# Performance work log

Measured on AMD Instinct MI355X. Metric: run time of the kernel, lower is better.

The kernel has to match this reference:

```python
import jax, jax.numpy as jnp
import numpy as np

N, E, IN, HID, HEADS, OUT = 50000, 800000, 128, 64, 4, 64


def setup_inputs() -> dict:
    key = jax.random.key(0)
    ks = jax.random.split(key, 13)
    s1 = 1.0 / np.sqrt(IN)
    s2 = 1.0 / np.sqrt(HID * HEADS)
    s3 = 1.0 / np.sqrt(HID)
    return {
        'x': jax.random.normal(ks[0], (N, IN), dtype=jnp.float32),
        'edge_index': jax.random.randint(ks[1], (2, E), 0, N, dtype=jnp.int64),
        # GATv2 layer 1: heads=HEADS, out=HID, concat=True
        'W1l': jax.random.normal(ks[2], (IN, HEADS * HID), dtype=jnp.float32) * s1,
        'W1r': jax.random.normal(ks[3], (IN, HEADS * HID), dtype=jnp.float32) * s1,
        'att1': jax.random.normal(ks[4], (HEADS, HID), dtype=jnp.float32) * s3,
        'b1': jnp.zeros((HEADS * HID,), dtype=jnp.float32),
        # GATv2 layer 2: heads=1, out=HID
        'W2l': jax.random.normal(ks[5], (HEADS * HID, HID), dtype=jnp.float32) * s2,
        'W2r': jax.random.normal(ks[6], (HEADS * HID, HID), dtype=jnp.float32) * s2,
        'att2': jax.random.normal(ks[7], (1, HID), dtype=jnp.float32) * s3,
        'b2': jnp.zeros((HID,), dtype=jnp.float32),
        # final Linear(HID, OUT)
        'Wlin': jax.random.normal(ks[8], (HID, OUT), dtype=jnp.float32) * s3,
        'blin': jnp.zeros((OUT,), dtype=jnp.float32),
    }


def _gatv2(x, src, dst, Wl, Wr, att, bias, n):
    # PyG GATv2Conv (share_weights=False): x_j -> lin_l, x_i -> lin_r
    H, C = att.shape
    xl = (x @ Wl).reshape(n, H, C)  # source transform [N,H,C]
    xr = (x @ Wr).reshape(n, H, C)  # destination transform [N,H,C]
    # per-edge GATv2 score: a^T LeakyReLU(xl_j + xr_i)
    e = jnp.sum(jax.nn.leaky_relu(xl[src] + xr[dst], 0.2) * att, axis=-1)  # [E,H]
    # scatter-softmax over edges sharing a destination
    m = jax.ops.segment_max(e, dst, num_segments=n)  # [N,H]
    ex = jnp.exp(e - m[dst])
    denom = jax.ops.segment_sum(ex, dst, num_segments=n)
    alpha = ex / (denom[dst] + 1e-16)  # [E,H]
    # weighted scatter-add aggregation of source features
    out = jax.ops.segment_sum(xl[src] * alpha[:, :, None], dst, num_segments=n)  # [N,H,C]
    return out.reshape(n, H * C) + bias


def reference(x, edge_index, W1l, W1r, att1, b1, W2l, W2r, att2, b2, Wlin, blin):
    n = x.shape[0]
    loops = jnp.arange(n, dtype=edge_index.dtype)
    src = jnp.concatenate([edge_index[0], loops])  # add_self_loops=True (PyG default)
    dst = jnp.concatenate([edge_index[1], loops])
    h = _gatv2(x, src, dst, W1l, W1r, att1, b1, n)
    h = jax.nn.elu(h)
    h = _gatv2(h, src, dst, W2l, W2r, att2, b2, n)
    h = jax.nn.elu(h)
    return h @ Wlin + blin
```

## Files before the change

kernel.cpp:

```cpp
#include <hip/hip_runtime.h>
#include <hip/hip_bf16.h>
#include <math.h>

#define N_NODES 50000
#define N_EDGES 800000
#define ETOT (N_EDGES + N_NODES)
#define NGRP 196
#define HBLK 416

typedef __attribute__((ext_vector_type(8))) short short8;
typedef __attribute__((ext_vector_type(4))) float floatx4;
typedef __attribute__((ext_vector_type(2))) float f32x2;

__device__ __forceinline__ float bf_lo(unsigned u) { return __uint_as_float(u << 16); }
__device__ __forceinline__ float bf_hi(unsigned u) { return __uint_as_float(u & 0xffff0000u); }
__device__ __forceinline__ unsigned short f2bf(float f) {
    unsigned u = __float_as_uint(f);
    return (unsigned short)((u + 0x7fffu + ((u >> 16) & 1u)) >> 16);
}
__device__ __forceinline__ unsigned pack2bf(float a, float b) {
    return (unsigned)f2bf(a) | ((unsigned)f2bf(b) << 16);
}
#define DPP_ADD(p, ctrl) \
    (p) += __int_as_float(__builtin_amdgcn_update_dpp(0, __float_as_int(p), (ctrl), 0xF, 0xF, true))

__global__ __launch_bounds__(256) void k_prep(const float* __restrict__ W1l,
                                              const float* __restrict__ W1r,
                                              const float* __restrict__ W2l,
                                              const float* __restrict__ W2r,
                                              const float* __restrict__ Wlin,
                                              unsigned short* __restrict__ Wt1,
                                              unsigned short* __restrict__ Wt2,
                                              unsigned short* __restrict__ Wt3,
                                              const int* __restrict__ ei,
                                              unsigned* __restrict__ part) {
    __shared__ unsigned sh[256];
    const int b = blockIdx.x;
    const int t = threadIdx.x;
    if (b < 400) {
        const int idx = b * 256 + t;
        if (idx < 65536) {
            const int k = idx >> 9;
            const int n = idx & 511;
            const float v = (n < 256) ? W1l[k * 256 + n] : W1r[k * 256 + (n - 256)];
            Wt1[n * 128 + k] = f2bf(v);
        } else if (idx < 98304) {
            const int j = idx - 65536;
            const int k = j >> 7;
            const int n = j & 127;
            const float v = (n < 64) ? W2l[k * 64 + n] : W2r[k * 64 + (n - 64)];
            Wt2[n * 256 + k] = f2bf(v);
        } else {
            const int j = idx - 98304;
            const int n = j >> 6, k = j & 63;
            Wt3[n * 64 + k] = f2bf(Wlin[k * 64 + n]);
        }
        return;
    }
    const int bb = b - 400;
    sh[t] = 0;
    __syncthreads();
#pragma unroll
    for (int j = 0; j < 8; j++) {
        const int e = bb * 2048 + j * 256 + t;
        if (e < ETOT) {
            const int d = (e < N_EDGES) ? ei[N_EDGES + e] : (e - N_EDGES);
            atomicAdd(&sh[d >> 8], 1u);
        }
    }
    __syncthreads();
    part[bb * 256 + t] = sh[t];
}

__global__ __launch_bounds__(256) void k_g1h(const float* __restrict__ x,
                                             const unsigned short* __restrict__ Wt1,
                                             unsigned short* __restrict__ xlb,
                                             unsigned short* __restrict__ xrb,
                                             const int* __restrict__ ei,
                                             const unsigned* __restrict__ part,
                                             int* __restrict__ g_off,
                                             unsigned* __restrict__ tmp) {
    __shared__ unsigned short sA[128 * 136];
    const int b = blockIdx.x;
    const int t = threadIdx.x;
    if (b >= 391) {
        __shared__ unsigned cur[256];
        __shared__ int wsum[4];
        const int bb = b - 391;
        const int lane = t & 63, wv = t >> 6;
        unsigned total_t = 0, base_t = 0;
        for (int b2 = 0; b2 < HBLK; b2++) {
            const unsigned v = part[b2 * 256 + t];
            total_t += v;
            base_t += (b2 < bb) ? v : 0u;
        }
        int incl = (int)total_t;
#pragma unroll
        for (int off = 1; off < 64; off <<= 1) {
            const int u = __shfl_up(incl, off);
            if (lane >= off) incl += u;
        }
        if (lane == 63) wsum[wv] = incl;
        __syncthreads();
        int woff = 0;
#pragma unroll
        for (int j = 0; j < 4; j++) woff += (j < wv) ? wsum[j] : 0;
        const int excl = incl - (int)total_t + woff;
        if (bb == 0) g_off[t] = excl;
        cur[t] = (unsigned)excl + base_t;
        __syncthreads();
#pragma unroll
        for (int j = 0; j < 8; j++) {
            const int e = bb * 2048 + j * 256 + t;
            if (e < ETOT) {
                int s, d;
                if (e < N_EDGES) { s = ei[e]; d = ei[N_EDGES + e]; }
                else { s = d = e - N_EDGES; }
                const unsigned item = ((unsigned)d << 16) | (unsigned)s;
                const unsigned pos = atomicAdd(&cur[d >> 8], 1u);
                tmp[pos] = item;
            }
        }
        return;
    }
    const int lane = t & 63, wv = t >> 6;
    const int m0 = b * 128;
#pragma unroll
    for (int j = 0; j < 16; j++) {
        const int i4 = t + j * 256;
        const int row = i4 >> 5, k4 = i4 & 31;
        float4 v = make_float4(0.f, 0.f, 0.f, 0.f);
        if (m0 + row < N_NODES) v = ((const float4*)x)[(long)(m0 + row) * 32 + k4];
        ushort4 u;
        u.x = f2bf(v.x); u.y = f2bf(v.y); u.z = f2bf(v.z); u.w = f2bf(v.w);
        *(ushort4*)&sA[row * 136 + k4 * 4] = u;
    }
    __syncthreads();
    const int l15 = lane & 15, quad = lane >> 4;
    const int nloc0 = wv * 64;
    for (int flavor = 0; flavor < 2; ++flavor) {
        unsigned short* outp = flavor ? xrb : xlb;
        short8 bfr[4][4];
#pragma unroll
        for (int nt = 0; nt < 4; nt++)
#pragma unroll
            for (int ks = 0; ks < 4; ks++)
                bfr[nt][ks] = *(const short8*)&Wt1[(flavor * 256 + nloc0 + nt * 16 + l15) * 128 + ks * 32 + quad * 8];
        for (int mt = 0; mt < 8; mt++) {
            short8 a[4];
#pragma unroll
            for (int ks = 0; ks < 4; ks++)
                a[ks] = *(const short8*)&sA[(mt * 16 + l15) * 136 + ks * 32 + quad * 8];
            floatx4 acc[4];
#pragma unroll
            for (int nt = 0; nt < 4; nt++) {
                acc[nt] = (floatx4)(0.f);
#pragma unroll
                for (int ks = 0; ks < 4; ks++)
                    acc[nt] = __builtin_amdgcn_mfma_f32_16x16x32_bf16(a[ks], bfr[nt][ks], acc[nt], 0, 0, 0);
            }
            const int mrow0 = m0 + mt * 16 + quad * 4;
#pragma unroll
            for (int nt = 0; nt < 4; nt++) {
                const int n = nloc0 + nt * 16 + l15;
#pragma unroll
                for (int r = 0; r < 4; r++) {
                    const int m = mrow0 + r;
                    if (m < N_NODES) outp[(long)m * 256 + n] = f2bf(acc[nt][r]);
                }
            }
        }
    }
}

__global__ __launch_bounds__(256) void k_bsort(const unsigned* __restrict__ tmp,
                                               const int* __restrict__ g_off,
                                               int* __restrict__ rowstart,
                                               int* __restrict__ deg,
                                               int* __restrict__ csr) {
    __shared__ unsigned h[256];
    __shared__ unsigned cur[256];
    __shared__ int wsum[4];
    const int t = threadIdx.x, lane = t & 63, wv = t >> 6;
    const int g = blockIdx.x;
    const int base = g_off[g];
    const int n = g_off[g + 1] - base;
    h[t] = 0;
    __syncthreads();
    for (int i = t; i < n; i += 256)
        atomicAdd(&h[(tmp[base + i] >> 16) & 255u], 1u);
    __syncthreads();
    const int v = (int)h[t];
    int incl = v;
#pragma unroll
    for (int off = 1; off < 64; off <<= 1) {
        const int u = __shfl_up(incl, off);
        if (lane >= off) incl += u;
    }
    if (lane == 63) wsum[wv] = incl;
    __syncthreads();
    int woff = 0;
#pragma unroll
    for (int j = 0; j < 4; j++) woff += (j < wv) ? wsum[j] : 0;
    const int excl = incl - v + woff;
    const int d = g * 256 + t;
    if (d < N_NODES) {
        rowstart[d] = base + excl;
        deg[d] = v;
    }
    cur[t] = (unsigned)excl;
    __syncthreads();
    for (int i = t; i < n; i += 256) {
        const unsigned item = tmp[base + i];
        const unsigned p = atomicAdd(&cur[(item >> 16) & 255u], 1u);
        csr[base + (int)p] = (int)((item & 0xFFFFu) << 9);
    }
}

__global__ __launch_bounds__(256) void k_node1(const int* __restrict__ rowstart,
                                               const int* __restrict__ deg,
                                               const int* __restrict__ csr,
                                               const uint4* __restrict__ xlb,
                                               const uint4* __restrict__ xrb,
                                               const float* __restrict__ att,
                                               const float* __restrict__ b1,
                                               uint4* __restrict__ h1b) {
    const int lane = threadIdx.x & 63;
    const int wv = threadIdx.x >> 6;
    const int node = blockIdx.x * 4 + wv;
    const int g = lane >> 5;
    const int l = lane & 31;
    const char* xlbase = (const char*)xlb;
    const uint4 xru = xrb[(long)node * 32 + l];
    const float4 ta = ((const float4*)att)[2 * l];
    const float4 tb = ((const float4*)att)[2 * l + 1];
    f32x2 xp[4], tp[4];
    xp[0] = (f32x2){bf_lo(xru.x), bf_hi(xru.x)};
    xp[1] = (f32x2){bf_lo(xru.y), bf_hi(xru.y)};
    xp[2] = (f32x2){bf_lo(xru.z), bf_hi(xru.z)};
    xp[3] = (f32x2){bf_lo(xru.w), bf_hi(xru.w)};
    tp[0] = (f32x2){ta.x, ta.y}; tp[1] = (f32x2){ta.z, ta.w};
    tp[2] = (f32x2){tb.x, tb.y}; tp[3] = (f32x2){tb.z, tb.w};
    const int start = rowstart[node];
    const int cnt = deg[node];
    const int ns = (cnt - g + 1) >> 1;
    float den = 0.f;
    f32x2 acc[4];
#pragma unroll
    for (int c = 0; c < 4; c++) acc[c] = (f32x2)(0.f);

    auto body = [&](const uint4& rr) {
        f32x2 a0, a1, a2, a3;
        a0.x = bf_lo(rr.x); a0.y = bf_hi(rr.x);
        a1.x = bf_lo(rr.y); a1.y = bf_hi(rr.y);
        a2.x = bf_lo(rr.z); a2.y = bf_hi(rr.z);
        a3.x = bf_lo(rr.w); a3.y = bf_hi(rr.w);
        f32x2 v = a0 + xp[0];
        f32x2 p2 = __builtin_elementwise_max(v, v * 0.2f) * tp[0];
        v = a1 + xp[1]; p2 += __builtin_elementwise_max(v, v * 0.2f) * tp[1];
        v = a2 + xp[2]; p2 += __builtin_elementwise_max(v, v * 0.2f) * tp[2];
        v = a3 + xp[3]; p2 += __builtin_elementwise_max(v, v * 0.2f) * tp[3];
        float p = p2.x + p2.y;
        DPP_ADD(p, 0xB1);
        DPP_ADD(p, 0x4E);
        DPP_ADD(p, 0x141);
        const float w = __expf(p);
        acc[0] += a0 * w;
        acc[1] += a1 * w;
        acc[2] += a2 * w;
        acc[3] += a3 * w;
        den += w;
    };

    uint4 rcur = make_uint4(0, 0, 0, 0), rnext = rcur;
    if (ns > 0) rcur = *((const uint4*)(xlbase + csr[start + g]) + l);
    if (ns > 1) rnext = *((const uint4*)(xlbase + csr[start + 2 + g]) + l);
    int i = 0;
    for (; i + 2 < ns; i++) {
        const uint4 r2 = *((const uint4*)(xlbase + csr[start + 2 * (i + 2) + g]) + l);
        body(rcur);
        rcur = rnext; rnext = r2;
    }
    for (; i < ns; i++) {
        body(rcur);
        rcur = rnext;
    }
    den += __shfl_xor(den, 32);
    const float inv = 1.f / (den + 1e-16f);
#pragma unroll
    for (int c = 0; c < 4; c++) {
        f32x2 t2 = acc[c];
        t2.x += __shfl_xor(t2.x, 32);
        t2.y += __shfl_xor(t2.y, 32);
        acc[c] = t2;
    }
    const float4 ba = ((const float4*)b1)[2 * l];
    const float4 bb = ((const float4*)b1)[2 * l + 1];
    f32x2 bp[4];
    bp[0] = (f32x2){ba.x, ba.y}; bp[1] = (f32x2){ba.z, ba.w};
    bp[2] = (f32x2){bb.x, bb.y}; bp[3] = (f32x2){bb.z, bb.w};
    float o[8];
#pragma unroll
    for (int c = 0; c < 4; c++) {
        f32x2 t2 = acc[c] * inv + bp[c];
        o[2 * c]     = t2.x > 0.f ? t2.x : expm1f(t2.x);
        o[2 * c + 1] = t2.y > 0.f ? t2.y : expm1f(t2.y);
    }
    if (g == 0) {
        uint4 u;
        u.x = pack2bf(o[0], o[1]);
        u.y = pack2bf(o[2], o[3]);
        u.z = pack2bf(o[4], o[5]);
        u.w = pack2bf(o[6], o[7]);
        h1b[(long)node * 32 + l] = u;
    }
}

__global__ __launch_bounds__(256) void k_gemm2(const uint4* __restrict__ h,
                                               const unsigned short* __restrict__ Wt2,
                                               unsigned short* __restrict__ xlb,
                                               unsigned short* __restrict__ xrb) {
    __shared__ unsigned short sA[64 * 264];
    const int t = threadIdx.x;
    const int lane = t & 63, wv = t >> 6;
    const int m0 = blockIdx.x * 64;
#pragma unroll
    for (int j = 0; j < 8; j++) {
        const int i8 = t + j * 256;
        const int row = i8 >> 5, c8 = i8 & 31;
        uint4 v = make_uint4(0, 0, 0, 0);
        if (m0 + row < N_NODES) v = h[(long)(m0 + row) * 32 + c8];
        *(uint4*)&sA[row * 264 + c8 * 8] = v;
    }
    __syncthreads();
    const int l15 = lane & 15, quad = lane >> 4;
    const int ncol0 = wv * 32;
    short8 b[2][8];
#pragma unroll
    for (int nt = 0; nt < 2; nt++)
#pragma unroll
        for (int ks = 0; ks < 8; ks++)
            b[nt][ks] = *(const short8*)&Wt2[(ncol0 + nt * 16 + l15) * 256 + ks * 32 + quad * 8];
    for (int mt = 0; mt < 4; mt++) {
        floatx4 acc[2];
        acc[0] = (floatx4)(0.f);
        acc[1] = (floatx4)(0.f);
#pragma unroll
        for (int ks = 0; ks < 8; ks++) {
            const short8 a = *(const short8*)&sA[(mt * 16 + l15) * 264 + ks * 32 + quad * 8];
            acc[0] = __builtin_amdgcn_mfma_f32_16x16x32_bf16(a, b[0][ks], acc[0], 0, 0, 0);
            acc[1] = __builtin_amdgcn_mfma_f32_16x16x32_bf16(a, b[1][ks], acc[1], 0, 0, 0);
        }
        const int mrow0 = m0 + mt * 16 + quad * 4;
#pragma unroll
        for (int nt = 0; nt < 2; nt++) {
            const int n = ncol0 + nt * 16 + l15;
#pragma unroll
            for (int r = 0; r < 4; r++) {
                const int m = mrow0 + r;
                if (m < N_NODES) {
                    if (n < 64) xlb[(long)m * 64 + n] = f2bf(acc[nt][r]);
                    else        xrb[(long)m * 64 + (n - 64)] = f2bf(acc[nt][r]);
                }
            }
        }
    }
}

__global__ __launch_bounds__(256) void k_node2(const int* __restrict__ rowstart,
                                               const int* __restrict__ deg,
                                               const int* __restrict__ csr,
                                               const uint2* __restrict__ xlb,
                                               const uint2* __restrict__ xrb,
                                               const float* __restrict__ att,
                                               const float* __restrict__ b2,
                                               const unsigned short* __restrict__ Wt3,
                                               const float* __restrict__ blin,
                                               float* __restrict__ out) {
    __shared__ unsigned short sH[16 * 72];
    const int lane = threadIdx.x & 63;
    const int wv = threadIdx.x >> 6;
    const int node = blockIdx.x * 4 + wv;
    const int g = lane >> 4;
    const int l = lane & 15;
    const char* xlbase = (const char*)xlb;
    const uint2 xru = xrb[(long)node * 16 + l];
    const float4 at4 = ((const float4*)att)[l];
    f32x2 xp[2], tp[2];
    xp[0] = (f32x2){bf_lo(xru.x), bf_hi(xru.x)};
    xp[1] = (f32x2){bf_lo(xru.y), bf_hi(xru.y)};
    tp[0] = (f32x2){at4.x, at4.y}; tp[1] = (f32x2){at4.z, at4.w};
    const int start = rowstart[node];
    const int cnt = deg[node];
    const int ns = (cnt - g + 3) >> 2;
    float den = 0.f;
    f32x2 acc[2];
    acc[0] = (f32x2)(0.f); acc[1] = (f32x2)(0.f);

    auto body = [&](const uint2& rr) {
        f32x2 a0, a1;
        a0.x = bf_lo(rr.x); a0.y = bf_hi(rr.x);
        a1.x = bf_lo(rr.y); a1.y = bf_hi(rr.y);
        f32x2 v = a0 + xp[0];
        f32x2 p2 = __builtin_elementwise_max(v, v * 0.2f) * tp[0];
        v = a1 + xp[1]; p2 += __builtin_elementwise_max(v, v * 0.2f) * tp[1];
        float p = p2.x + p2.y;
        DPP_ADD(p, 0xB1);
        DPP_ADD(p, 0x4E);
        DPP_ADD(p, 0x141);
        DPP_ADD(p, 0x140);
        const float w = __expf(p);
        acc[0] += a0 * w;
        acc[1] += a1 * w;
        den += w;
    };

    uint2 rcur = make_uint2(0, 0), rnext = rcur;
    if (ns > 0) rcur = *((const uint2*)(xlbase + (csr[start + g] >> 2)) + l);
    if (ns > 1) rnext = *((const uint2*)(xlbase + (csr[start + 4 + g] >> 2)) + l);
    int i = 0;
    for (; i + 2 < ns; i++) {
        const uint2 r2 = *((const uint2*)(xlbase + (csr[start + 4 * (i + 2) + g] >> 2)) + l);
        body(rcur);
        rcur = rnext; rnext = r2;
    }
    for (; i < ns; i++) {
        body(rcur);
        rcur = rnext;
    }
    den += __shfl_xor(den, 16);
    den += __shfl_xor(den, 32);
    const float inv = 1.f / (den + 1e-16f);
    float t0 = acc[0].x, t1 = acc[0].y, t2 = acc[1].x, t3 = acc[1].y;
    t0 += __shfl_xor(t0, 16); t0 += __shfl_xor(t0, 32);
    t1 += __shfl_xor(t1, 16); t1 += __shfl_xor(t1, 32);
    t2 += __shfl_xor(t2, 16); t2 += __shfl_xor(t2, 32);
    t3 += __shfl_xor(t3, 16); t3 += __shfl_xor(t3, 32);
    const float4 b4 = ((const float4*)b2)[l];
    float4 h4;
    h4.x = t0 * inv + b4.x; h4.x = h4.x > 0.f ? h4.x : expm1f(h4.x);
    h4.y = t1 * inv + b4.y; h4.y = h4.y > 0.f ? h4.y : expm1f(h4.y);
    h4.z = t2 * inv + b4.z; h4.z = h4.z > 0.f ? h4.z : expm1f(h4.z);
    h4.w = t3 * inv + b4.w; h4.w = h4.w > 0.f ? h4.w : expm1f(h4.w);
    for (int idx = threadIdx.x; idx < 16 * 72; idx += 256) sH[idx] = 0;
    __syncthreads();
    if (g == 0) {
        *(uint2*)&sH[wv * 72 + 4 * l] =
            make_uint2(pack2bf(h4.x, h4.y), pack2bf(h4.z, h4.w));
    }
    __syncthreads();
    const int l15 = lane & 15, quad = lane >> 4;
    const int n0 = wv * 16;
    const short8 a0  = *(const short8*)&sH[l15 * 72 + quad * 8];
    const short8 a1  = *(const short8*)&sH[l15 * 72 + 32 + quad * 8];
    const short8 bb0 = *(const short8*)&Wt3[(n0 + l15) * 64 + quad * 8];
    const short8 bb1 = *(const short8*)&Wt3[(n0 + l15) * 64 + 32 + quad * 8];
    floatx4 acc2 = (floatx4)(0.f);
    acc2 = __builtin_amdgcn_mfma_f32_16x16x32_bf16(a0, bb0, acc2, 0, 0, 0);
    acc2 = __builtin_amdgcn_mfma_f32_16x16x32_bf16(a1, bb1, acc2, 0, 0, 0);
    if (quad == 0) {
        const float bl = blin[n0 + l15];
        const long node0 = (long)blockIdx.x * 4;
#pragma unroll
        for (int r = 0; r < 4; r++)
            out[(node0 + r) * 64 + n0 + l15] = acc2[r] + bl;
    }
}

extern "C" void kernel_launch(void* const* d_in, const int* in_sizes, int n_in,
                              void* d_out, int out_size, void* d_ws, size_t ws_size,
                              hipStream_t stream) {
    (void)in_sizes; (void)n_in; (void)out_size; (void)ws_size;
    const float* x    = (const float*)d_in[0];
    const int*   ei   = (const int*)d_in[1];
    const float* W1l  = (const float*)d_in[2];
    const float* W1r  = (const float*)d_in[3];
    const float* att1 = (const float*)d_in[4];
    const float* b1   = (const float*)d_in[5];
    const float* W2l  = (const float*)d_in[6];
    const float* W2r  = (const float*)d_in[7];
    const float* att2 = (const float*)d_in[8];
    const float* b2   = (const float*)d_in[9];
    const float* Wlin = (const float*)d_in[10];
    const float* blin = (const float*)d_in[11];

    float* ws = (float*)d_ws;
    unsigned short* XL1b = (unsigned short*)(ws);
    unsigned short* XR1b = (unsigned short*)(ws + 6400000);
    uint4*          H1b  = (uint4*)(ws + 12800000);
    unsigned*       tmp  = (unsigned*)(ws + 12800000);
    unsigned*       part = (unsigned*)(ws + 14000000);
    unsigned short* XL2b = (unsigned short*)(ws + 19200000);
    unsigned short* XR2b = (unsigned short*)(ws + 20800000);
    int* deg       = (int*)(ws + 22400000);
    int* rowstart  = (int*)(ws + 22450000);
    int* csr       = (int*)(ws + 22550000);
    int* g_off     = (int*)(ws + 23430000);
    unsigned short* Wt1 = (unsigned short*)(ws + 23500000);
    unsigned short* Wt2 = (unsigned short*)(ws + 23550000);
    unsigned short* Wt3 = (unsigned short*)(ws + 23600000);

    k_prep<<<400 + HBLK, 256, 0, stream>>>(W1l, W1r, W2l, W2r, Wlin,
                                           Wt1, Wt2, Wt3, ei, part);
    k_g1h<<<391 + HBLK, 256, 0, stream>>>(x, Wt1, XL1b, XR1b, ei, part, g_off, tmp);
    k_bsort<<<NGRP, 256, 0, stream>>>(tmp, g_off, rowstart, deg, csr);
    k_node1<<<12500, 256, 0, stream>>>(rowstart, deg, csr,
                                       (const uint4*)XL1b, (const uint4*)XR1b,
                                       att1, b1, H1b);
    k_gemm2<<<782, 256, 0, stream>>>((const uint4*)H1b, Wt2, XL2b, XR2b);
    k_node2<<<12500, 256, 0, stream>>>(rowstart, deg, csr,
                                       (const uint2*)XL2b, (const uint2*)XR2b,
                                       att2, b2, Wt3, blin, (float*)d_out);
}
```

Measured before the change: 275.5 us.

## Fuse layer-2 projection GEMM into layer-1 node aggregation kernel

```diff
diff --git a/kernel.cpp b/kernel.cpp
--- a/kernel.cpp
+++ b/kernel.cpp
@@ -217,14 +217,17 @@
     }
 }
 
-__global__ __launch_bounds__(256) void k_node1(const int* __restrict__ rowstart,
-                                               const int* __restrict__ deg,
-                                               const int* __restrict__ csr,
-                                               const uint4* __restrict__ xlb,
-                                               const uint4* __restrict__ xrb,
-                                               const float* __restrict__ att,
-                                               const float* __restrict__ b1,
-                                               uint4* __restrict__ h1b) {
+__global__ __launch_bounds__(256, 8) void k_node1(const int* __restrict__ rowstart,
+                                                  const int* __restrict__ deg,
+                                                  const int* __restrict__ csr,
+                                                  const uint4* __restrict__ xlb,
+                                                  const uint4* __restrict__ xrb,
+                                                  const float* __restrict__ att,
+                                                  const float* __restrict__ b1,
+                                                  const unsigned short* __restrict__ Wt2,
+                                                  unsigned short* __restrict__ xl2,
+                                                  unsigned short* __restrict__ xr2) {
+    __shared__ unsigned short sH[16 * 264];
     const int lane = threadIdx.x & 63;
     const int wv = threadIdx.x >> 6;
     const int node = blockIdx.x * 4 + wv;
@@ -312,57 +315,36 @@
         u.y = pack2bf(o[2], o[3]);
         u.z = pack2bf(o[4], o[5]);
         u.w = pack2bf(o[6], o[7]);
-        h1b[(long)node * 32 + l] = u;
-    }
-}
-
-__global__ __launch_bounds__(256) void k_gemm2(const uint4* __restrict__ h,
-                                               const unsigned short* __restrict__ Wt2,
-                                               unsigned short* __restrict__ xlb,
-                                               unsigned short* __restrict__ xrb) {
-    __shared__ unsigned short sA[64 * 264];
-    const int t = threadIdx.x;
-    const int lane = t & 63, wv = t >> 6;
-    const int m0 = blockIdx.x * 64;
-#pragma unroll
-    for (int j = 0; j < 8; j++) {
-        const int i8 = t + j * 256;
-        const int row = i8 >> 5, c8 = i8 & 31;
-        uint4 v = make_uint4(0, 0, 0, 0);
-        if (m0 + row < N_NODES) v = h[(long)(m0 + row) * 32 + c8];
-        *(uint4*)&sA[row * 264 + c8 * 8] = v;
+        *(uint4*)&sH[wv * 264 + l * 8] = u;
+    }
+    {
+        uint4 z = make_uint4(0, 0, 0, 0);
+        uint4* zp = (uint4*)&sH[4 * 264];
+        for (int idx = threadIdx.x; idx < 396; idx += 256) zp[idx] = z;
     }
     __syncthreads();
     const int l15 = lane & 15, quad = lane >> 4;
     const int ncol0 = wv * 32;
-    short8 b[2][8];
-#pragma unroll
-    for (int nt = 0; nt < 2; nt++)
-#pragma unroll
-        for (int ks = 0; ks < 8; ks++)
-            b[nt][ks] = *(const short8*)&Wt2[(ncol0 + nt * 16 + l15) * 256 + ks * 32 + quad * 8];
-    for (int mt = 0; mt < 4; mt++) {
-        floatx4 acc[2];
-        acc[0] = (floatx4)(0.f);
-        acc[1] = (floatx4)(0.f);
-#pragma unroll
-        for (int ks = 0; ks < 8; ks++) {
-            const short8 a = *(const short8*)&sA[(mt * 16 + l15) * 264 + ks * 32 + quad * 8];
-            acc[0] = __builtin_amdgcn_mfma_f32_16x16x32_bf16(a, b[0][ks], acc[0], 0, 0, 0);
-            acc[1] = __builtin_amdgcn_mfma_f32_16x16x32_bf16(a, b[1][ks], acc[1], 0, 0, 0);
-        }
-        const int mrow0 = m0 + mt * 16 + quad * 4;
-#pragma unroll
-        for (int nt = 0; nt < 2; nt++) {
-            const int n = ncol0 + nt * 16 + l15;
-#pragma unroll
-            for (int r = 0; r < 4; r++) {
-                const int m = mrow0 + r;
-                if (m < N_NODES) {
-                    if (n < 64) xlb[(long)m * 64 + n] = f2bf(acc[nt][r]);
-                    else        xrb[(long)m * 64 + (n - 64)] = f2bf(acc[nt][r]);
-                }
-            }
+    floatx4 c0 = (floatx4)(0.f), c1 = (floatx4)(0.f);
+#pragma unroll 2
+    for (int ks = 0; ks < 8; ks++) {
+        const short8 a  = *(const short8*)&sH[l15 * 264 + ks * 32 + quad * 8];
+        const short8 w0 = *(const short8*)&Wt2[(ncol0 + l15) * 256 + ks * 32 + quad * 8];
+        const short8 w1 = *(const short8*)&Wt2[(ncol0 + 16 + l15) * 256 + ks * 32 + quad * 8];
+        c0 = __builtin_amdgcn_mfma_f32_16x16x32_bf16(a, w0, c0, 0, 0, 0);
+        c1 = __builtin_amdgcn_mfma_f32_16x16x32_bf16(a, w1, c1, 0, 0, 0);
+    }
+    if (quad == 0) {
+        const long node0 = (long)blockIdx.x * 4;
+        const int n0 = ncol0 + l15;
+        const int n1 = ncol0 + 16 + l15;
+#pragma unroll
+        for (int r = 0; r < 4; r++) {
+            const long m = node0 + r;
+            const unsigned short v0 = f2bf(c0[r]);
+            const unsigned short v1 = f2bf(c1[r]);
+            if (n0 < 64) xl2[m * 64 + n0] = v0; else xr2[m * 64 + (n0 - 64)] = v0;
+            if (n1 < 64) xl2[m * 64 + n1] = v1; else xr2[m * 64 + (n1 - 64)] = v1;
         }
     }
 }
@@ -487,7 +469,6 @@
     float* ws = (float*)d_ws;
     unsigned short* XL1b = (unsigned short*)(ws);
     unsigned short* XR1b = (unsigned short*)(ws + 6400000);
-    uint4*          H1b  = (uint4*)(ws + 12800000);
     unsigned*       tmp  = (unsigned*)(ws + 12800000);
     unsigned*       part = (unsigned*)(ws + 14000000);
     unsigned short* XL2b = (unsigned short*)(ws + 19200000);
@@ -506,8 +487,7 @@
     k_bsort<<<NGRP, 256, 0, stream>>>(tmp, g_off, rowstart, deg, csr);
     k_node1<<<12500, 256, 0, stream>>>(rowstart, deg, csr,
                                        (const uint4*)XL1b, (const uint4*)XR1b,
-                                       att1, b1, H1b);
-    k_gemm2<<<782, 256, 0, stream>>>((const uint4*)H1b, Wt2, XL2b, XR2b);
+                                       att1, b1, Wt2, XL2b, XR2b);
     k_node2<<<12500, 256, 0, stream>>>(rowstart, deg, csr,
                                        (const uint2*)XL2b, (const uint2*)XR2b,
                                        att2, b2, Wt3, blin, (float*)d_out);
```

Result: slower. 316.9 us (+15.0%).
